# Optimization experiments

Hardware: AMD Instinct MI355X
Metric: run time of the kernel (lower is better)

The kernel has to match this reference:

```python
import jax, jax.numpy as jnp
import numpy as np

N_NODES = 100000
N_EDGES = 3200000
IN_CH = 512
HID = 16
OUT_CH = 2


def setup_inputs() -> dict:
    key = jax.random.key(0)
    k1, k2, k3, k4 = jax.random.split(key, 4)
    x = jax.random.normal(k1, (N_NODES, IN_CH), dtype=jnp.float32)
    edge_index = jax.random.randint(k2, (2, N_EDGES), 0, N_NODES, dtype=jnp.int32)
    # GCNConv weight (glorot-style scale) and zero bias; Linear xavier weight, zero bias
    W1 = jax.random.normal(k3, (IN_CH, HID), dtype=jnp.float32) * np.float32(np.sqrt(2.0 / (IN_CH + HID)))
    b1 = jnp.zeros((HID,), dtype=jnp.float32)
    W2 = jax.random.normal(k4, (HID, OUT_CH), dtype=jnp.float32) * np.float32(np.sqrt(2.0 / (HID + OUT_CH)))
    b2 = jnp.zeros((OUT_CH,), dtype=jnp.float32)
    return {"x": x, "edge_index": edge_index, "W1": W1, "b1": b1, "W2": W2, "b2": b2}


def reference(x, edge_index, W1, b1, W2, b2):
    # GCNConv with default add_self_loops=True, normalize=True:
    #   out = D^{-1/2} (A + I) D^{-1/2} X W1 + b1, then Linear(16, out).
    n = x.shape[0]
    loops = jnp.arange(n, dtype=edge_index.dtype)
    row = jnp.concatenate([edge_index[0], loops])  # source nodes j
    col = jnp.concatenate([edge_index[1], loops])  # target nodes i
    deg = jax.ops.segment_sum(jnp.ones_like(col, dtype=x.dtype), col, num_segments=n)
    dinv = jnp.where(deg > 0, jax.lax.rsqrt(deg), jnp.zeros_like(deg))
    norm = dinv[row] * dinv[col]  # [E+N]
    xw = x @ W1  # [N, 16] project first (PyG GCNConv order)
    agg = jax.ops.segment_sum(xw[row] * norm[:, None], col, num_segments=n)  # scatter-add to targets
    h = agg + b1
    return h @ W2 + b2  # [N, out_channels]
```

## Files before the change

### kernel.cpp

```cpp
#include <hip/hip_runtime.h>


constexpr int N_NODES = 100000;
constexpr int N_EDGES = 3200000;
constexpr int IN_CH   = 512;
constexpr int HID     = 16;
constexpr int OUT_CH  = 2;

constexpr int NBUCK = (N_NODES + 255) / 256;
constexpr int BIN_BLOCKS = 320;
constexpr int EPB = N_EDGES / BIN_BLOCKS;

typedef __attribute__((ext_vector_type(4))) float floatx4;


__global__ __launch_bounds__(256) void k_wc(const float* __restrict__ W1,
                                            const float* __restrict__ b1,
                                            const float* __restrict__ W2,
                                            const float* __restrict__ b2,
                                            float* __restrict__ Wc,
                                            float* __restrict__ bconst) {
    int i = blockIdx.x * 256 + threadIdx.x;
    int c = i >> 1, o = i & 1;
    float s = 0.f;
#pragma unroll
    for (int h = 0; h < HID; ++h) s += W1[c * HID + h] * W2[h * OUT_CH + o];
    Wc[i] = s;
    if (i < OUT_CH) {
        float bo = b2[i];
#pragma unroll
        for (int h = 0; h < HID; ++h) bo += b1[h] * W2[h * OUT_CH + i];
        bconst[i] = bo;
    }
}

__global__ __launch_bounds__(256) void k_count(const int* __restrict__ tgt,
                                               int* __restrict__ cnt) {
    __shared__ int hist[NBUCK];
    for (int i = threadIdx.x; i < NBUCK; i += 256) hist[i] = 0;
    __syncthreads();
    int e0 = blockIdx.x * EPB;
    for (int e = e0 + threadIdx.x; e < e0 + EPB; e += 256)
        atomicAdd(&hist[tgt[e] >> 8], 1);
    __syncthreads();
    for (int i = threadIdx.x; i < NBUCK; i += 256)
        if (hist[i]) atomicAdd(&cnt[i], hist[i]);
}

__global__ __launch_bounds__(512) void k_scan(const int* __restrict__ cnt,
                                              int* __restrict__ base,
                                              int* __restrict__ cursor) {
    __shared__ int tmp[512];
    int tid = threadIdx.x;
    int v = (tid < NBUCK) ? cnt[tid] : 0;
    tmp[tid] = v;
    __syncthreads();
#pragma unroll
    for (int off = 1; off < 512; off <<= 1) {
        int tv = (tid >= off) ? tmp[tid - off] : 0;
        __syncthreads();
        tmp[tid] += tv;
        __syncthreads();
    }
    if (tid < NBUCK) { int b = tmp[tid] - v; base[tid] = b; cursor[tid] = b; }
    if (tid == NBUCK - 1) base[NBUCK] = tmp[tid];
}

__global__ __launch_bounds__(256) void k_bin(const int* __restrict__ ei,
                                             int* __restrict__ cursor,
                                             int* __restrict__ binned) {
    __shared__ int hist[NBUCK];
    __shared__ int lbase[NBUCK];
    __shared__ int lcur[NBUCK];
    for (int i = threadIdx.x; i < NBUCK; i += 256) { hist[i] = 0; lcur[i] = 0; }
    __syncthreads();
    int e0 = blockIdx.x * EPB;
    int e1 = e0 + EPB;
    for (int e = e0 + threadIdx.x; e < e1; e += 256)
        atomicAdd(&hist[ei[N_EDGES + e] >> 8], 1);
    __syncthreads();
    for (int i = threadIdx.x; i < NBUCK; i += 256)
        lbase[i] = hist[i] ? atomicAdd(&cursor[i], hist[i]) : 0;
    __syncthreads();
    for (int e = e0 + threadIdx.x; e < e1; e += 256) {
        int tg = ei[N_EDGES + e];
        int b = tg >> 8;
        int off = atomicAdd(&lcur[b], 1);
        binned[lbase[b] + off] = ((tg & 255) << 20) | ei[e];
    }
}

__global__ __launch_bounds__(256) void k_dinv(const int* __restrict__ base,
                                              const int* __restrict__ binned,
                                              float* __restrict__ dinv) {
    __shared__ int cnt[256];
    cnt[threadIdx.x] = 0;
    __syncthreads();
    int b = blockIdx.x;
    int s = base[b], e = base[b + 1];
    for (int i = s + threadIdx.x; i < e; i += 256)
        atomicAdd(&cnt[binned[i] >> 20], 1);
    __syncthreads();
    int node = (b << 8) + threadIdx.x;
    if (node < N_NODES)
        dinv[node] = rsqrtf((float)(cnt[threadIdx.x] + 1));
}

__global__ __launch_bounds__(256) void k_xw(const float* __restrict__ x,
                                            const float* __restrict__ Wc,
                                            const float* __restrict__ dinv,
                                            float2* __restrict__ t) {
    int node = (blockIdx.x * 256 + threadIdx.x) >> 6;
    int lane = threadIdx.x & 63;
    const floatx4* xr = reinterpret_cast<const floatx4*>(
        x + (size_t)node * IN_CH + lane * 8);
    const floatx4* wr = reinterpret_cast<const floatx4*>(Wc + lane * 16);
    floatx4 x0 = xr[0], x1 = xr[1];
    floatx4 w0 = wr[0], w1 = wr[1], w2 = wr[2], w3 = wr[3];
    float s0 = x0[0]*w0[0] + x0[1]*w0[2] + x0[2]*w1[0] + x0[3]*w1[2]
             + x1[0]*w2[0] + x1[1]*w2[2] + x1[2]*w3[0] + x1[3]*w3[2];
    float s1 = x0[0]*w0[1] + x0[1]*w0[3] + x0[2]*w1[1] + x0[3]*w1[3]
             + x1[0]*w2[1] + x1[1]*w2[3] + x1[2]*w3[1] + x1[3]*w3[3];
    s0 += __shfl_xor(s0, 32); s1 += __shfl_xor(s1, 32);
    s0 += __shfl_xor(s0, 16); s1 += __shfl_xor(s1, 16);
    s0 += __shfl_xor(s0, 8);  s1 += __shfl_xor(s1, 8);
    s0 += __shfl_xor(s0, 4);  s1 += __shfl_xor(s1, 4);
    s0 += __shfl_xor(s0, 2);  s1 += __shfl_xor(s1, 2);
    s0 += __shfl_xor(s0, 1);  s1 += __shfl_xor(s1, 1);
    if (lane == 0) {
        float di = dinv[node];
        t[node] = make_float2(di * s0, di * s1);
    }
}

__global__ __launch_bounds__(256) void k_acc(const int* __restrict__ base,
                                             const int* __restrict__ binned,
                                             const float2* __restrict__ t,
                                             const float* __restrict__ dinv,
                                             const float* __restrict__ bconst,
                                             float2* __restrict__ out) {
    __shared__ float acc0[256];
    __shared__ float acc1[256];
    acc0[threadIdx.x] = 0.f;
    acc1[threadIdx.x] = 0.f;
    __syncthreads();
    int b = blockIdx.x;
    int s = base[b], e = base[b + 1];
    for (int i = s + threadIdx.x; i < e; i += 256) {
        int v = binned[i];
        int local = v >> 20;
        int src = v & 0xFFFFF;
        float2 ts = t[src];
        atomicAdd(&acc0[local], ts.x);
        atomicAdd(&acc1[local], ts.y);
    }
    __syncthreads();
    int node = (b << 8) + threadIdx.x;
    if (node < N_NODES) {
        float2 self = t[node];
        float di = dinv[node];
        out[node] = make_float2(di * (acc0[threadIdx.x] + self.x) + bconst[0],
                                di * (acc1[threadIdx.x] + self.y) + bconst[1]);
    }
}

extern "C" void kernel_launch(void* const* d_in, const int* in_sizes, int n_in,
                              void* d_out, int out_size, void* d_ws, size_t ws_size,
                              hipStream_t stream) {
    const float* x  = (const float*)d_in[0];
    const int*   ei = (const int*)d_in[1];
    const float* W1 = (const float*)d_in[2];
    const float* b1 = (const float*)d_in[3];
    const float* W2 = (const float*)d_in[4];
    const float* b2 = (const float*)d_in[5];

    char* ws = (char*)d_ws;
    float*  Wc     = (float*) (ws + 0);
    float*  bconst = (float*) (ws + 4096);
    int*    cnt    = (int*)   (ws + 4608);
    int*    basep  = (int*)   (ws + 6400);
    int*    cursor = (int*)   (ws + 8192);
    float*  dinv   = (float*) (ws + 16384);
    float2* t      = (float2*)(ws + 416384);
    int*    binned = (int*)   (ws + 1216384);

    hipMemsetAsync(cnt, 0, NBUCK * sizeof(int), stream);

    k_wc   <<<4, 256, 0, stream>>>(W1, b1, W2, b2, Wc, bconst);
    k_count<<<BIN_BLOCKS, 256, 0, stream>>>(ei + N_EDGES, cnt);
    k_scan <<<1, 512, 0, stream>>>(cnt, basep, cursor);
    k_bin  <<<BIN_BLOCKS, 256, 0, stream>>>(ei, cursor, binned);
    k_dinv <<<NBUCK, 256, 0, stream>>>(basep, binned, dinv);
    k_xw   <<<(N_NODES * 64) / 256, 256, 0, stream>>>(x, Wc, dinv, t);
    k_acc  <<<NBUCK, 256, 0, stream>>>(basep, binned, t, dinv, bconst,
                                       (float2*)d_out);
}
```

Measured before the change: 441.1 us.

## Merge binning with X·W projection and use per-block histogram scan

Replaces global atomic bucket counting with per-block histograms written to memory, a column-wise exclusive scan, and a bucket-base scan, so binning no longer needs a histogram recount or global cursor atomics. The binning work and the dense x·Wc projection now run in one launch as separate block ranges, so the edge-scatter blocks can overlap with the bandwidth-heavy projection of x. The dinv scaling of t moves into the degree kernel, which removes the dependency that forced the projection to wait for degrees. This adds an extra read-modify-write pass over t and two small scan launches, and drops the memset and k_wc launches.

```diff
diff --git a/kernel.cpp b/kernel.cpp
--- a/kernel.cpp
+++ b/kernel.cpp
@@ -7,52 +7,80 @@
 constexpr int HID     = 16;
 constexpr int OUT_CH  = 2;
 
-constexpr int NBUCK = (N_NODES + 255) / 256;
+constexpr int NBUCK      = (N_NODES + 255) / 256;
 constexpr int BIN_BLOCKS = 320;
-constexpr int EPB = N_EDGES / BIN_BLOCKS;
+constexpr int EPB        = N_EDGES / BIN_BLOCKS;
+constexpr int XW_BLOCKS  = N_NODES / 4;
 
 typedef __attribute__((ext_vector_type(4))) float floatx4;
 
 
-__global__ __launch_bounds__(256) void k_wc(const float* __restrict__ W1,
-                                            const float* __restrict__ b1,
-                                            const float* __restrict__ W2,
-                                            const float* __restrict__ b2,
-                                            float* __restrict__ Wc,
-                                            float* __restrict__ bconst) {
-    int i = blockIdx.x * 256 + threadIdx.x;
-    int c = i >> 1, o = i & 1;
-    float s = 0.f;
-#pragma unroll
-    for (int h = 0; h < HID; ++h) s += W1[c * HID + h] * W2[h * OUT_CH + o];
-    Wc[i] = s;
-    if (i < OUT_CH) {
-        float bo = b2[i];
-#pragma unroll
-        for (int h = 0; h < HID; ++h) bo += b1[h] * W2[h * OUT_CH + i];
-        bconst[i] = bo;
-    }
-}
-
-__global__ __launch_bounds__(256) void k_count(const int* __restrict__ tgt,
-                                               int* __restrict__ cnt) {
-    __shared__ int hist[NBUCK];
-    for (int i = threadIdx.x; i < NBUCK; i += 256) hist[i] = 0;
+__global__ __launch_bounds__(256) void k_count_wc(const int* __restrict__ tgt,
+                                                  int* __restrict__ hist,
+                                                  const float* __restrict__ W1,
+                                                  const float* __restrict__ b1,
+                                                  const float* __restrict__ W2,
+                                                  const float* __restrict__ b2,
+                                                  float* __restrict__ Wc,
+                                                  float* __restrict__ bconst) {
+    if (blockIdx.x == BIN_BLOCKS) {
+        for (int i = threadIdx.x; i < IN_CH * OUT_CH; i += 256) {
+            int c = i >> 1, o = i & 1;
+            float s = 0.f;
+#pragma unroll
+            for (int h = 0; h < HID; ++h) s += W1[c * HID + h] * W2[h * OUT_CH + o];
+            Wc[i] = s;
+        }
+        if (threadIdx.x < OUT_CH) {
+            float bo = b2[threadIdx.x];
+#pragma unroll
+            for (int h = 0; h < HID; ++h) bo += b1[h] * W2[h * OUT_CH + threadIdx.x];
+            bconst[threadIdx.x] = bo;
+        }
+        return;
+    }
+    __shared__ int h[NBUCK];
+    for (int i = threadIdx.x; i < NBUCK; i += 256) h[i] = 0;
     __syncthreads();
     int e0 = blockIdx.x * EPB;
     for (int e = e0 + threadIdx.x; e < e0 + EPB; e += 256)
-        atomicAdd(&hist[tgt[e] >> 8], 1);
+        atomicAdd(&h[tgt[e] >> 8], 1);
     __syncthreads();
     for (int i = threadIdx.x; i < NBUCK; i += 256)
-        if (hist[i]) atomicAdd(&cnt[i], hist[i]);
-}
-
-__global__ __launch_bounds__(512) void k_scan(const int* __restrict__ cnt,
-                                              int* __restrict__ base,
-                                              int* __restrict__ cursor) {
+        hist[blockIdx.x * NBUCK + i] = h[i];
+}
+
+__global__ __launch_bounds__(64) void k_colscan(int* __restrict__ hist,
+                                                int* __restrict__ coltot) {
+    int b = blockIdx.x;
+    int lane = threadIdx.x;
+    int v[5];
+    int s = 0;
+#pragma unroll
+    for (int j = 0; j < 5; ++j) {
+        v[j] = hist[(lane * 5 + j) * NBUCK + b];
+        s += v[j];
+    }
+    int inc = s;
+#pragma unroll
+    for (int off = 1; off < 64; off <<= 1) {
+        int n = __shfl_up(inc, off);
+        if (lane >= off) inc += n;
+    }
+    int excl = inc - s;
+#pragma unroll
+    for (int j = 0; j < 5; ++j) {
+        hist[(lane * 5 + j) * NBUCK + b] = excl;
+        excl += v[j];
+    }
+    if (lane == 63) coltot[b] = inc;
+}
+
+__global__ __launch_bounds__(512) void k_basescan(const int* __restrict__ coltot,
+                                                  int* __restrict__ bbase) {
     __shared__ int tmp[512];
     int tid = threadIdx.x;
-    int v = (tid < NBUCK) ? cnt[tid] : 0;
+    int v = (tid < NBUCK) ? coltot[tid] : 0;
     tmp[tid] = v;
     __syncthreads();
 #pragma unroll
@@ -62,55 +90,34 @@
         tmp[tid] += tv;
         __syncthreads();
     }
-    if (tid < NBUCK) { int b = tmp[tid] - v; base[tid] = b; cursor[tid] = b; }
-    if (tid == NBUCK - 1) base[NBUCK] = tmp[tid];
-}
-
-__global__ __launch_bounds__(256) void k_bin(const int* __restrict__ ei,
-                                             int* __restrict__ cursor,
-                                             int* __restrict__ binned) {
-    __shared__ int hist[NBUCK];
-    __shared__ int lbase[NBUCK];
-    __shared__ int lcur[NBUCK];
-    for (int i = threadIdx.x; i < NBUCK; i += 256) { hist[i] = 0; lcur[i] = 0; }
-    __syncthreads();
-    int e0 = blockIdx.x * EPB;
-    int e1 = e0 + EPB;
-    for (int e = e0 + threadIdx.x; e < e1; e += 256)
-        atomicAdd(&hist[ei[N_EDGES + e] >> 8], 1);
-    __syncthreads();
-    for (int i = threadIdx.x; i < NBUCK; i += 256)
-        lbase[i] = hist[i] ? atomicAdd(&cursor[i], hist[i]) : 0;
-    __syncthreads();
-    for (int e = e0 + threadIdx.x; e < e1; e += 256) {
-        int tg = ei[N_EDGES + e];
-        int b = tg >> 8;
-        int off = atomicAdd(&lcur[b], 1);
-        binned[lbase[b] + off] = ((tg & 255) << 20) | ei[e];
-    }
-}
-
-__global__ __launch_bounds__(256) void k_dinv(const int* __restrict__ base,
-                                              const int* __restrict__ binned,
-                                              float* __restrict__ dinv) {
-    __shared__ int cnt[256];
-    cnt[threadIdx.x] = 0;
-    __syncthreads();
-    int b = blockIdx.x;
-    int s = base[b], e = base[b + 1];
-    for (int i = s + threadIdx.x; i < e; i += 256)
-        atomicAdd(&cnt[binned[i] >> 20], 1);
-    __syncthreads();
-    int node = (b << 8) + threadIdx.x;
-    if (node < N_NODES)
-        dinv[node] = rsqrtf((float)(cnt[threadIdx.x] + 1));
-}
-
-__global__ __launch_bounds__(256) void k_xw(const float* __restrict__ x,
-                                            const float* __restrict__ Wc,
-                                            const float* __restrict__ dinv,
-                                            float2* __restrict__ t) {
-    int node = (blockIdx.x * 256 + threadIdx.x) >> 6;
+    if (tid < NBUCK) bbase[tid] = tmp[tid] - v;
+    if (tid == NBUCK - 1) bbase[NBUCK] = tmp[tid];
+}
+
+__global__ __launch_bounds__(256) void k_bin_xw(const int* __restrict__ ei,
+                                                int* __restrict__ hist,
+                                                const int* __restrict__ bbase,
+                                                int* __restrict__ binned,
+                                                const float* __restrict__ x,
+                                                const float* __restrict__ Wc,
+                                                float2* __restrict__ t2) {
+    if (blockIdx.x < BIN_BLOCKS) {
+        __shared__ int lcur[NBUCK];
+        int blk = blockIdx.x;
+        for (int i = threadIdx.x; i < NBUCK; i += 256)
+            lcur[i] = bbase[i] + hist[blk * NBUCK + i];
+        __syncthreads();
+        int e0 = blk * EPB;
+        for (int e = e0 + threadIdx.x; e < e0 + EPB; e += 256) {
+            int tg = ei[N_EDGES + e];
+            int b = tg >> 8;
+            int pos = atomicAdd(&lcur[b], 1);
+            binned[pos] = ((tg & 255) << 20) | ei[e];
+        }
+        return;
+    }
+    int nb = blockIdx.x - BIN_BLOCKS;
+    int node = nb * 4 + (threadIdx.x >> 6);
     int lane = threadIdx.x & 63;
     const floatx4* xr = reinterpret_cast<const floatx4*>(
         x + (size_t)node * IN_CH + lane * 8);
@@ -127,15 +134,33 @@
     s0 += __shfl_xor(s0, 4);  s1 += __shfl_xor(s1, 4);
     s0 += __shfl_xor(s0, 2);  s1 += __shfl_xor(s1, 2);
     s0 += __shfl_xor(s0, 1);  s1 += __shfl_xor(s1, 1);
-    if (lane == 0) {
-        float di = dinv[node];
-        t[node] = make_float2(di * s0, di * s1);
-    }
-}
-
-__global__ __launch_bounds__(256) void k_acc(const int* __restrict__ base,
+    if (lane == 0) t2[node] = make_float2(s0, s1);
+}
+
+__global__ __launch_bounds__(256) void k_dinv(const int* __restrict__ bbase,
+                                              const int* __restrict__ binned,
+                                              float* __restrict__ dinv,
+                                              float2* __restrict__ t2) {
+    __shared__ int cnt[256];
+    cnt[threadIdx.x] = 0;
+    __syncthreads();
+    int b = blockIdx.x;
+    int s = bbase[b], e = bbase[b + 1];
+    for (int i = s + threadIdx.x; i < e; i += 256)
+        atomicAdd(&cnt[binned[i] >> 20], 1);
+    __syncthreads();
+    int node = (b << 8) + threadIdx.x;
+    if (node < N_NODES) {
+        float di = rsqrtf((float)(cnt[threadIdx.x] + 1));
+        dinv[node] = di;
+        float2 v = t2[node];
+        t2[node] = make_float2(v.x * di, v.y * di);
+    }
+}
+
+__global__ __launch_bounds__(256) void k_acc(const int* __restrict__ bbase,
                                              const int* __restrict__ binned,
-                                             const float2* __restrict__ t,
+                                             const float2* __restrict__ t2,
                                              const float* __restrict__ dinv,
                                              const float* __restrict__ bconst,
                                              float2* __restrict__ out) {
@@ -145,19 +170,17 @@
     acc1[threadIdx.x] = 0.f;
     __syncthreads();
     int b = blockIdx.x;
-    int s = base[b], e = base[b + 1];
+    int s = bbase[b], e = bbase[b + 1];
     for (int i = s + threadIdx.x; i < e; i += 256) {
         int v = binned[i];
-        int local = v >> 20;
-        int src = v & 0xFFFFF;
-        float2 ts = t[src];
-        atomicAdd(&acc0[local], ts.x);
-        atomicAdd(&acc1[local], ts.y);
+        float2 ts = t2[v & 0xFFFFF];
+        atomicAdd(&acc0[v >> 20], ts.x);
+        atomicAdd(&acc1[v >> 20], ts.y);
     }
     __syncthreads();
     int node = (b << 8) + threadIdx.x;
     if (node < N_NODES) {
-        float2 self = t[node];
+        float2 self = t2[node];
         float di = dinv[node];
         out[node] = make_float2(di * (acc0[threadIdx.x] + self.x) + bconst[0],
                                 di * (acc1[threadIdx.x] + self.y) + bconst[1]);
@@ -175,23 +198,22 @@
     const float* b2 = (const float*)d_in[5];
 
     char* ws = (char*)d_ws;
-    float*  Wc     = (float*) (ws + 0);
-    float*  bconst = (float*) (ws + 4096);
-    int*    cnt    = (int*)   (ws + 4608);
-    int*    basep  = (int*)   (ws + 6400);
-    int*    cursor = (int*)   (ws + 8192);
-    float*  dinv   = (float*) (ws + 16384);
-    float2* t      = (float2*)(ws + 416384);
-    int*    binned = (int*)   (ws + 1216384);
-
-    hipMemsetAsync(cnt, 0, NBUCK * sizeof(int), stream);
-
-    k_wc   <<<4, 256, 0, stream>>>(W1, b1, W2, b2, Wc, bconst);
-    k_count<<<BIN_BLOCKS, 256, 0, stream>>>(ei + N_EDGES, cnt);
-    k_scan <<<1, 512, 0, stream>>>(cnt, basep, cursor);
-    k_bin  <<<BIN_BLOCKS, 256, 0, stream>>>(ei, cursor, binned);
-    k_dinv <<<NBUCK, 256, 0, stream>>>(basep, binned, dinv);
-    k_xw   <<<(N_NODES * 64) / 256, 256, 0, stream>>>(x, Wc, dinv, t);
-    k_acc  <<<NBUCK, 256, 0, stream>>>(basep, binned, t, dinv, bconst,
-                                       (float2*)d_out);
-}
+    int*    hist   = (int*)   (ws + 0);
+    int*    coltot = (int*)   (ws + 500480);
+    int*    bbase  = (int*)   (ws + 502048);
+    float*  Wc     = (float*) (ws + 503616);
+    float*  bconst = (float*) (ws + 507712);
+    float*  dinv   = (float*) (ws + 507728);
+    float2* t2     = (float2*)(ws + 907728);
+    int*    binned = (int*)   (ws + 1707728);
+
+    k_count_wc<<<BIN_BLOCKS + 1, 256, 0, stream>>>(ei + N_EDGES, hist,
+                                                   W1, b1, W2, b2, Wc, bconst);
+    k_colscan <<<NBUCK, 64, 0, stream>>>(hist, coltot);
+    k_basescan<<<1, 512, 0, stream>>>(coltot, bbase);
+    k_bin_xw  <<<BIN_BLOCKS + XW_BLOCKS, 256, 0, stream>>>(ei, hist, bbase,
+                                                           binned, x, Wc, t2);
+    k_dinv    <<<NBUCK, 256, 0, stream>>>(bbase, binned, dinv, t2);
+    k_acc     <<<NBUCK, 256, 0, stream>>>(bbase, binned, t2, dinv, bconst,
+                                          (float2*)d_out);
+}
```

After: 413.4 us. 6.3% less time.
